# Optimization experiments

Hardware: AMD Instinct MI355X
Metric: run time of the kernel (lower is better)

## Reference

```python
import jax, jax.numpy as jnp
import numpy as np

# dims
B, T, D, H, DFF, NTYPE = 8, 1024, 512, 8, 1024, 341
HD = D // H                    # 64 head dim
NUM_AXES = 1
DPR = D // H // (NUM_AXES + 1) # 32 dims rotated per axis
EPS = 1e-5
THETA = 10000.0


def layernorm(x, g, b):
    m = jnp.mean(x, axis=-1, keepdims=True)
    v = jnp.mean((x - m) ** 2, axis=-1, keepdims=True)
    return (x - m) * jax.lax.rsqrt(v + EPS) * g + b


def swiglu(x):
    a, gate = jnp.split(x, 2, axis=-1)
    return jax.nn.silu(gate) * a


def apply_rope(x, pos):
    # x: [B,H,T,DPR], pos: [B,T] float positions (possibly non-integer / scrambled order)
    inv_freq = 1.0 / (THETA ** (jnp.arange(0, DPR, 2, dtype=jnp.float32) / DPR))  # [DPR/2]
    freqs = pos[:, None, :, None] * inv_freq          # [B,1,T,DPR/2]
    cos = jnp.repeat(jnp.cos(freqs), 2, axis=-1)      # each freq repeated twice -> [B,1,T,DPR]
    sin = jnp.repeat(jnp.sin(freqs), 2, axis=-1)
    x1 = x[..., 0::2]
    x2 = x[..., 1::2]
    rot = jnp.stack([-x2, x1], axis=-1).reshape(x.shape)  # rotate_half, interleaved pairs
    return x * cos + rot * sin


def setup_inputs() -> dict:
    key = jax.random.key(0)
    ks = jax.random.split(key, 16)
    s = lambda d: 1.0 / np.sqrt(d)
    return {
        "x_type": jax.random.randint(ks[0], (B, T + 1), 0, NTYPE),
        "x_value": jax.random.normal(ks[1], (B, T, D), dtype=jnp.float32),
        "seq_order": jax.random.uniform(ks[2], (B, T + 1), dtype=jnp.float32) * T,
        "W_attn": jax.random.normal(ks[3], (D, 3 * D), dtype=jnp.float32) * s(D),
        "type_emb": jax.random.normal(ks[4], (NTYPE, 2 * D), dtype=jnp.float32) * 0.02,
        "ln1_g": jnp.ones((D,), jnp.float32),
        "ln1_b": jnp.zeros((D,), jnp.float32),
        "ln2_g": jnp.ones((D,), jnp.float32),
        "ln2_b": jnp.zeros((D,), jnp.float32),
        "W1": jax.random.normal(ks[5], (D, 2 * DFF), dtype=jnp.float32) * s(D),
        "b1": jnp.zeros((2 * DFF,), jnp.float32),
        "W2": jax.random.normal(ks[6], (DFF, D), dtype=jnp.float32) * s(DFF),
        "b2": jnp.zeros((D,), jnp.float32),
    }


def reference(x_type, x_value, seq_order, W_attn, type_emb, ln1_g, ln1_b, ln2_g, ln2_b, W1, b1, W2, b2):
    # --- attention sublayer ---
    h = layernorm(x_value, ln1_g, ln1_b)                  # [B,T,D]
    qkv = h @ W_attn                                      # [B,T,3D]
    q, k, v = jnp.split(qkv, 3, axis=-1)
    emb = type_emb[x_type]                                # [B,T+1,2D]
    q_embed, k_embed = jnp.split(emb, 2, axis=-1)
    q = q + q_embed[:, :-1]
    k = k + k_embed[:, 1:]
    # [B,H,T,HD]
    to_heads = lambda t: t.reshape(B, T, H, HD).transpose(0, 2, 1, 3)
    q, k, v = to_heads(q), to_heads(k), to_heads(v)
    # rotate first DPR dims with (shifted) seq_order; remaining dims untouched
    q = jnp.concatenate([apply_rope(q[..., :DPR], seq_order[:, :-1]), q[..., DPR:]], axis=-1)
    k = jnp.concatenate([apply_rope(k[..., :DPR], seq_order[:, 1:]), k[..., DPR:]], axis=-1)
    # causal SDPA
    scores = jnp.einsum("bhqd,bhkd->bhqk", q, k) / jnp.sqrt(jnp.float32(HD))
    causal = jnp.tril(jnp.ones((T, T), dtype=bool))
    scores = jnp.where(causal, scores, -jnp.inf)
    attn = jax.nn.softmax(scores, axis=-1)
    out = jnp.einsum("bhqk,bhkd->bhqd", attn, v)          # [B,H,T,HD]
    out = out.transpose(0, 2, 1, 3).reshape(B, T, D)
    x = x_value + out
    # --- SwiGLU FFN sublayer ---
    h2 = layernorm(x, ln2_g, ln2_b)
    ff = swiglu(h2 @ W1 + b1) @ W2 + b2
    return x + ff
```

## Files before the change

### kernel.cpp

```cpp
#include <hip/hip_runtime.h>
#include <stdint.h>
#include <math.h>

typedef unsigned short u16;
typedef unsigned int u32;
typedef __attribute__((ext_vector_type(8))) short bf16x8;
typedef __attribute__((ext_vector_type(4))) float f32x4;
typedef __attribute__((ext_vector_type(2))) float f32x2;
typedef __attribute__((ext_vector_type(2))) u16 u16x2;
typedef __attribute__((ext_vector_type(8))) u16 u16x8;
typedef __attribute__((ext_vector_type(2))) u32 u32x2;

#define B_ 8
#define T_ 1024
#define D_ 512
#define H_ 8
#define TP1 1025
#define QSCALE 0.1803368801111204f

__device__ __forceinline__ u16 f2b(float f) {
  union { float f; u32 u; } v; v.f = f;
  return (u16)((v.u + 0x7fffu + ((v.u >> 16) & 1u)) >> 16);
}
__device__ __forceinline__ void gld16(const void* g, void* l) {
  __builtin_amdgcn_global_load_lds((const __attribute__((address_space(1))) u32*)g,
                                   (__attribute__((address_space(3))) u32*)l, 16, 0, 0);
}
__device__ __forceinline__ f32x4 mfma16(bf16x8 a, bf16x8 b, f32x4 c) {
  return __builtin_amdgcn_mfma_f32_16x16x32_bf16(a, b, c, 0, 0, 0);
}
__device__ __forceinline__ u32 cvtpk(float lo, float hi) {
  u32 r;
  asm("v_cvt_pk_bf16_f32 %0, %1, %2" : "=v"(r) : "v"(lo), "v"(hi));
  return r;
}
union U8 { u32 u[4]; bf16x8 v; };

#define WAITV(N) asm volatile("s_waitcnt vmcnt(" #N ")" ::: "memory")

__global__ __launch_bounds__(256) void prep_kernel(const float* __restrict__ W_attn,
    const float* __restrict__ W1, const float* __restrict__ W2,
    const float* __restrict__ seq,
    u16* __restrict__ WtA, u16* __restrict__ W1i, u16* __restrict__ W2t,
    float* __restrict__ cq, float* __restrict__ sq_,
    float* __restrict__ ck, float* __restrict__ sk,
    const float* __restrict__ xv, const float* __restrict__ ln1g,
    const float* __restrict__ ln1b, u16* __restrict__ hbuf) {
  int bid = blockIdx.x, tid = threadIdx.x;
  if (bid >= 1088) {
    int row = (bid - 1088) * 4 + (tid >> 6);
    int lane = tid & 63;
    const float* xr = xv + (size_t)row * D_ + lane * 8;
    f32x4 v0 = *(const f32x4*)xr;
    f32x4 v1 = *(const f32x4*)(xr + 4);
    float s = 0.f, sq = 0.f;
    #pragma unroll
    for (int j = 0; j < 4; j++) { s += v0[j] + v1[j]; sq += v0[j] * v0[j] + v1[j] * v1[j]; }
    #pragma unroll
    for (int m = 1; m < 64; m <<= 1) { s += __shfl_xor(s, m); sq += __shfl_xor(sq, m); }
    float mean = s * (1.f / D_);
    float var = sq * (1.f / D_) - mean * mean;
    float rstd = rsqrtf(var + 1e-5f);
    f32x4 g0 = *(const f32x4*)(ln1g + lane * 8);
    f32x4 g1 = *(const f32x4*)(ln1g + lane * 8 + 4);
    f32x4 b0 = *(const f32x4*)(ln1b + lane * 8);
    f32x4 b1 = *(const f32x4*)(ln1b + lane * 8 + 4);
    u16x8 o;
    #pragma unroll
    for (int j = 0; j < 4; j++) {
      o[j]     = f2b((v0[j] - mean) * rstd * g0[j] + b0[j]);
      o[4 + j] = f2b((v1[j] - mean) * rstd * g1[j] + b1[j]);
    }
    *(u16x8*)(hbuf + (size_t)row * D_ + lane * 8) = o;
    return;
  }
  if (bid >= 576) {
    int i = (bid - 576) * 256 + tid;
    int p = i & 15, bt = i >> 4, b = bt >> 10, t = bt & 1023;
    float inv = expf(-(float)p * 0.5756462732485115f);
    float aq = seq[b * TP1 + t] * inv;
    float ak = seq[b * TP1 + t + 1] * inv;
    cq[i] = cosf(aq); sq_[i] = sinf(aq);
    ck[i] = cosf(ak); sk[i] = sinf(ak);
    return;
  }
  __shared__ u16 lt[64][65];
  const float* src; u16* dst; int ld, Kd, k0, r0; bool ilv = false;
  if (bid < 192) {
    src = W_attn; dst = WtA; ld = 1536; Kd = 512;
    k0 = (bid & 7) * 64; r0 = (bid >> 3) * 64;
  } else if (bid < 448) {
    int t = bid - 192;
    src = W1; dst = W1i; ld = 2048; Kd = 512; ilv = true;
    k0 = (t & 7) * 64; r0 = (t >> 3) * 64;
  } else {
    int t = bid - 448;
    src = W2; dst = W2t; ld = 512; Kd = 1024;
    k0 = (t & 15) * 64; r0 = (t >> 4) * 64;
  }
  int nl = tid & 63;
  int scol, rloc;
  if (ilv) {
    if (nl < 32) { scol = (r0 >> 1) + nl;          rloc = ((nl >> 4) << 5) + (nl & 15); }
    else         { scol = 1024 + (r0 >> 1) + (nl - 32); rloc = (((nl - 32) >> 4) << 5) + 16 + (nl & 15); }
  } else { scol = r0 + nl; rloc = nl; }
  #pragma unroll
  for (int it = 0; it < 16; it++) {
    int kl = (tid >> 6) * 16 + it;
    lt[rloc][kl] = f2b(src[(size_t)(k0 + kl) * ld + scol]);
  }
  __syncthreads();
  #pragma unroll
  for (int it = 0; it < 16; it++) {
    int rl = (tid >> 6) * 16 + it;
    dst[(size_t)(r0 + rl) * Kd + k0 + nl] = lt[rl][nl];
  }
}

__global__ __launch_bounds__(256) void ln_kernel(const float* __restrict__ x,
    const float* __restrict__ g, const float* __restrict__ bta, u16* __restrict__ out) {
  int row = blockIdx.x * 4 + (threadIdx.x >> 6);
  int lane = threadIdx.x & 63;
  const float* xr = x + (size_t)row * D_ + lane * 8;
  f32x4 v0 = *(const f32x4*)xr;
  f32x4 v1 = *(const f32x4*)(xr + 4);
  float s = 0.f, sq = 0.f;
  #pragma unroll
  for (int j = 0; j < 4; j++) { s += v0[j] + v1[j]; sq += v0[j] * v0[j] + v1[j] * v1[j]; }
  #pragma unroll
  for (int m = 1; m < 64; m <<= 1) { s += __shfl_xor(s, m); sq += __shfl_xor(sq, m); }
  float mean = s * (1.f / D_);
  float var = sq * (1.f / D_) - mean * mean;
  float rstd = rsqrtf(var + 1e-5f);
  f32x4 g0 = *(const f32x4*)(g + lane * 8);
  f32x4 g1 = *(const f32x4*)(g + lane * 8 + 4);
  f32x4 b0 = *(const f32x4*)(bta + lane * 8);
  f32x4 b1 = *(const f32x4*)(bta + lane * 8 + 4);
  u16x8 o;
  #pragma unroll
  for (int j = 0; j < 4; j++) {
    o[j]     = f2b((v0[j] - mean) * rstd * g0[j] + b0[j]);
    o[4 + j] = f2b((v1[j] - mean) * rstd * g1[j] + b1[j]);
  }
  *(u16x8*)(out + (size_t)row * D_ + lane * 8) = o;
}

__global__ __launch_bounds__(256) void gemm_qkv(const u16* __restrict__ A,
    const u16* __restrict__ Bt,
    const int* __restrict__ x_type, const float* __restrict__ type_emb,
    const float* __restrict__ rqc, const float* __restrict__ rqs,
    const float* __restrict__ rkc, const float* __restrict__ rks,
    u16* __restrict__ qT, u16* __restrict__ kT, u16* __restrict__ vT) {
  __shared__ u16 lsmem[6 * 4096];
  u16* lA = lsmem;
  u16* lB = lsmem + 3 * 4096;
  const int K = 512, NK = 16;
  const int tid = threadIdx.x, lane = tid & 63, w = tid >> 6;
  const int wm = w >> 1, wn = w & 1;
  int swz = (blockIdx.x & 7) * 96 + (blockIdx.x >> 3);
  int byy = swz / 12, bxx = swz - byy * 12;
  const size_t bm = (size_t)byy * 128;
  const size_t bn = (size_t)bxx * 128;

  const int r0 = tid >> 2;
  const int cs = ((tid & 3) ^ ((r0 >> 1) & 3)) * 8;
  const u16* a0 = A + (bm + r0) * K + cs;
  const u16* a1 = A + (bm + 64 + r0) * K + cs;
  const u16* b0 = Bt + (bn + r0) * K + cs;
  const u16* b1p = Bt + (bn + 64 + r0) * K + cs;

  int aoff[4], boff[4];
  #pragma unroll
  for (int i = 0; i < 4; i++) {
    int ra = wm * 64 + i * 16 + (lane & 15);
    aoff[i] = ra * 64 + (((lane >> 4) ^ ((ra >> 1) & 3)) * 16);
    int rb = wn * 64 + i * 16 + (lane & 15);
    boff[i] = rb * 64 + (((lane >> 4) ^ ((rb >> 1) & 3)) * 16);
  }

  auto stage = [&](int j, int buf) {
    char* ad = (char*)lA + buf * 8192 + w * 1024;
    char* bd = (char*)lB + buf * 8192 + w * 1024;
    gld16(a0 + j * 32, ad);
    gld16(a1 + j * 32, ad + 4096);
    gld16(b0 + j * 32, bd);
    gld16(b1p + j * 32, bd + 4096);
  };
  f32x4 acc[4][4] = {};
  auto compute = [&](int buf) {
    const char* lAc = (const char*)lA + buf * 8192;
    const char* lBc = (const char*)lB + buf * 8192;
    bf16x8 af[4], bf[4];
    #pragma unroll
    for (int i = 0; i < 4; i++) af[i] = *(const bf16x8*)(lAc + aoff[i]);
    #pragma unroll
    for (int n = 0; n < 4; n++) bf[n] = *(const bf16x8*)(lBc + boff[n]);
    __builtin_amdgcn_s_setprio(1);
    #pragma unroll
    for (int i = 0; i < 4; i++)
      #pragma unroll
      for (int n = 0; n < 4; n++)
        acc[i][n] = mfma16(af[i], bf[n], acc[i][n]);
    __builtin_amdgcn_s_setprio(0);
  };

  stage(0, 0);
  stage(1, 1);
  int cur = 0;
  for (int j = 0; j < NK - 1; j++) {
    WAITV(4);
    __builtin_amdgcn_s_barrier();
    if (j + 2 < NK) { int nb = cur + 2; if (nb >= 3) nb -= 3; stage(j + 2, nb); }
    compute(cur);
    cur = (cur + 1 == 3) ? 0 : cur + 1;
  }
  WAITV(0);
  __builtin_amdgcn_s_barrier();
  compute(cur);

  const int region = (int)(bn >> 9);
  __syncthreads();
  u16 (*tbuf)[136] = (u16(*)[136])lsmem;
  const int bb = (int)(bm >> 10);
  const int t0 = (int)(bm & 1023);

  if (region < 2) {
    #pragma unroll
    for (int i = 0; i < 4; i++) {
      #pragma unroll
      for (int jj = 0; jj < 4; jj++) {
        int rl = wm * 64 + i * 16 + (lane >> 4) * 4 + jj;
        int row = (int)bm + rl;
        int b = row >> 10, t = row & 1023;
        int ty = x_type[b * TP1 + t + region];
        const float* rc = (region == 0) ? rqc : rkc;
        const float* rs = (region == 0) ? rqs : rks;
        #pragma unroll
        for (int n = 0; n < 4; n++) {
          int cl = wn * 64 + n * 16 + (lane & 15);
          int cloc = ((int)bn - region * 512) + cl;
          int hd = cloc & 63;
          float v = acc[i][n][jj] + type_emb[(size_t)ty * 1024 + region * 512 + cloc];
          float vp = __shfl_xor(v, 1);
          if (hd < 32) {
            int p = hd >> 1;
            float c = rc[row * 16 + p], s = rs[row * 16 + p];
            v = (hd & 1) ? (v * c + vp * s) : (v * c - vp * s);
          }
          if (region == 0) v *= QSCALE;
          tbuf[rl][cl] = f2b(v);
        }
      }
    }
    __syncthreads();
    u16* dst = (region == 0) ? qT : kT;
    const int h0 = (((int)bn - region * 512) >> 6);
    #pragma unroll
    for (int p = 0; p < 8; p++) {
      int chunk = p * 256 + tid;
      int tl = chunk >> 4;
      int cc = (chunk & 15) * 8;
      u16x8 o = *(const u16x8*)&tbuf[tl][cc];
      *(u16x8*)(dst + ((size_t)(bb * 8 + h0 + (cc >> 6)) * T_ + t0 + tl) * 64 +
                (cc & 63)) = o;
    }
  } else {
    #pragma unroll
    for (int i = 0; i < 4; i++) {
      #pragma unroll
      for (int n = 0; n < 4; n++) {
        int cl = wn * 64 + n * 16 + (lane & 15);
        #pragma unroll
        for (int jj = 0; jj < 4; jj++) {
          int r = wm * 64 + i * 16 + (lane >> 4) * 4 + jj;
          tbuf[cl][r] = f2b(acc[i][n][jj]);
        }
      }
    }
    __syncthreads();
    const int h0 = ((int)bn - 1024) >> 6;
    const size_t rbase = (size_t)(bb * 8 + h0) * 64;
    #pragma unroll
    for (int p = 0; p < 8; p++) {
      int rl = p * 16 + (tid >> 4);
      int c8 = (tid & 15) * 8;
      u16x8 o = *(const u16x8*)&tbuf[rl][c8];
      *(u16x8*)(vT + (rbase + rl) * T_ + t0 + c8) = o;
    }
  }
}

__global__ __launch_bounds__(512) void gemm_ff1(const u16* __restrict__ A,
    const u16* __restrict__ Bt, const float* __restrict__ b1,
    u16* __restrict__ outp) {
  __shared__ u16 lsmem[24576];
  u16* lA = lsmem;
  u16* lB = lsmem + 16384;
  const int K = 512;
  const int tid = threadIdx.x, lane = tid & 63, w = tid >> 6;
  const int wm = w >> 2, wn = w & 3;
  int swz = (blockIdx.x & 7) * 64 + (blockIdx.x >> 3);
  int byy = swz >> 4, bxx = swz & 15;
  const size_t bm = (size_t)byy * 256;
  const size_t bn = (size_t)bxx * 128;

  const int r0 = tid >> 2;
  const int cs = ((tid & 3) ^ ((r0 >> 1) & 3)) * 8;
  const u16* a0 = A + (bm + r0) * K + cs;
  const u16* a1 = A + (bm + 128 + r0) * K + cs;
  const u16* b0 = Bt + (bn + r0) * K + cs;

  int aoff[8], boff[2];
  #pragma unroll
  for (int i = 0; i < 8; i++) {
    int ra = wm * 128 + i * 16 + (lane & 15);
    aoff[i] = ra * 64 + (((lane >> 4) ^ ((ra >> 1) & 3)) * 16);
  }
  #pragma unroll
  for (int n = 0; n < 2; n++) {
    int rb = wn * 32 + n * 16 + (lane & 15);
    boff[n] = rb * 64 + (((lane >> 4) ^ ((rb >> 1) & 3)) * 16);
  }

  auto stage = [&](int k0, int buf) {
    char* ad = (char*)lA + buf * 16384 + w * 1024;
    char* bd = (char*)lB + buf * 8192 + w * 1024;
    gld16(a0 + k0, ad);
    gld16(a1 + k0, ad + 8192);
    gld16(b0 + k0, bd);
  };

  f32x4 acc[8][2] = {};
  stage(0, 0);
  __syncthreads();
  int cur = 0;
  for (int k0 = 0; k0 < K; k0 += 32) {
    if (k0 + 32 < K) stage(k0 + 32, cur ^ 1);
    const char* lAc = (const char*)lA + cur * 16384;
    const char* lBc = (const char*)lB + cur * 8192;
    bf16x8 bf[2];
    #pragma unroll
    for (int n = 0; n < 2; n++) bf[n] = *(const bf16x8*)(lBc + boff[n]);
    __builtin_amdgcn_s_setprio(1);
    #pragma unroll
    for (int i = 0; i < 8; i++) {
      bf16x8 af = *(const bf16x8*)(lAc + aoff[i]);
      acc[i][0] = mfma16(af, bf[0], acc[i][0]);
      acc[i][1] = mfma16(af, bf[1], acc[i][1]);
    }
    __builtin_amdgcn_s_setprio(0);
    __syncthreads();
    cur ^= 1;
  }
  __syncthreads();
  u16 (*tbuf)[72] = (u16(*)[72])lsmem;
  {
    int cl = wn * 16 + (lane & 15);
    int c = ((int)bn >> 1) + cl;
    float bav = b1[c], bgv = b1[1024 + c];
    #pragma unroll
    for (int i = 0; i < 8; i++) {
      #pragma unroll
      for (int jj = 0; jj < 4; jj++) {
        int rl = wm * 128 + i * 16 + (lane >> 4) * 4 + jj;
        float av = acc[i][0][jj] + bav;
        float gv = acc[i][1][jj] + bgv;
        float sg = gv / (1.f + expf(-gv));
        tbuf[rl][cl] = f2b(sg * av);
      }
    }
  }
  __syncthreads();
  {
    const int c0 = ((int)bn >> 1);
    #pragma unroll
    for (int p = 0; p < 4; p++) {
      int ch = p * 512 + tid;
      int rl = ch >> 3;
      int cc = (ch & 7) * 8;
      u16x8 o = *(const u16x8*)&tbuf[rl][cc];
      *(u16x8*)(outp + (size_t)((int)bm + rl) * 1024 + c0 + cc) = o;
    }
  }
}

__global__ __launch_bounds__(512) void gemm_ff2(const u16* __restrict__ A,
    const u16* __restrict__ Bt, const float* __restrict__ bias,
    float* __restrict__ C) {
  __shared__ u16 lA[2][8192];
  __shared__ u16 lB[2][8192];
  const int K = 1024, N = 512, NJ = 16;
  const int tid = threadIdx.x, lane = tid & 63, w = tid >> 6;
  const int wm = w >> 2, wn = w & 3;
  int swz = (blockIdx.x & 7) * 32 + (blockIdx.x >> 3);
  int byy = swz >> 2, bxx = swz & 3;
  const size_t bm = (size_t)byy * 128;
  const size_t bn = (size_t)bxx * 128;

  const int r0 = tid >> 2;
  const int cs = ((tid & 3) ^ ((r0 >> 1) & 3)) * 8;
  const u16* a0 = A + (bm + r0) * K + cs;
  const u16* b0 = Bt + (bn + r0) * K + cs;

  int aoff[4], boff[2];
  #pragma unroll
  for (int i = 0; i < 4; i++) {
    int ra = wm * 64 + i * 16 + (lane & 15);
    aoff[i] = ra * 64 + (((lane >> 4) ^ ((ra >> 1) & 3)) * 16);
  }
  #pragma unroll
  for (int n = 0; n < 2; n++) {
    int rb = wn * 32 + n * 16 + (lane & 15);
    boff[n] = rb * 64 + (((lane >> 4) ^ ((rb >> 1) & 3)) * 16);
  }

  auto stage = [&](int j, int buf) {
    #pragma unroll
    for (int kh = 0; kh < 2; kh++) {
      int ko = j * 64 + kh * 32;
      gld16(a0 + ko, (char*)lA + buf * 16384 + kh * 8192 + w * 1024);
      gld16(b0 + ko, (char*)lB + buf * 16384 + kh * 8192 + w * 1024);
    }
  };
  f32x4 acc[4][2] = {};
  auto compute = [&](int buf) {
    #pragma unroll
    for (int kh = 0; kh < 2; kh++) {
      const char* lAc = (const char*)lA + buf * 16384 + kh * 8192;
      const char* lBc = (const char*)lB + buf * 16384 + kh * 8192;
      bf16x8 af[4], bf[2];
      #pragma unroll
      for (int i = 0; i < 4; i++) af[i] = *(const bf16x8*)(lAc + aoff[i]);
      #pragma unroll
      for (int n = 0; n < 2; n++) bf[n] = *(const bf16x8*)(lBc + boff[n]);
      __builtin_amdgcn_s_setprio(1);
      #pragma unroll
      for (int i = 0; i < 4; i++)
        #pragma unroll
        for (int n = 0; n < 2; n++)
          acc[i][n] = mfma16(af[i], bf[n], acc[i][n]);
      __builtin_amdgcn_s_setprio(0);
    }
  };

  stage(0, 0);
  __syncthreads();
  int cur = 0;
  for (int j = 0; j < NJ; j++) {
    if (j + 1 < NJ) stage(j + 1, cur ^ 1);
    compute(cur);
    __syncthreads();
    cur ^= 1;
  }

  #pragma unroll
  for (int i = 0; i < 4; i++) {
    size_t mrow = bm + wm * 64 + i * 16 + (lane >> 4) * 4;
    #pragma unroll
    for (int n = 0; n < 2; n++) {
      size_t col = bn + wn * 32 + n * 16 + (lane & 15);
      float bv = bias[col];
      #pragma unroll
      for (int jj = 0; jj < 4; jj++) {
        size_t idx = (mrow + jj) * (size_t)N + col;
        C[idx] = acc[i][n][jj] + bv + C[idx];
      }
    }
  }
}

__global__ __launch_bounds__(512, 4) void attn_kernel(const u16* __restrict__ qT,
    const u16* __restrict__ kT, const u16* __restrict__ vT,
    const float* __restrict__ xv, float* __restrict__ X) {
  int s0 = (blockIdx.x & 7) * 64 + (blockIdx.x >> 3);
  const int bh = ((blockIdx.x & 7) << 3) + (s0 & 7);
  const int qp = 7 - ((s0 >> 3) & 7);
  const int b = bh >> 3, h = bh & 7;
  const int tid = threadIdx.x, lane = tid & 63, w = tid >> 6;
  const int q = lane & 15, g = lane >> 4;
  __shared__ u16 lK[2][8192];
  __shared__ u16 lV[2][8192];

  const int qrow0 = qp * 128 + w * 16;
  bf16x8 qf[2];
  {
    const u16* qp_ = qT + ((size_t)bh * T_ + qrow0 + q) * 64 + g * 8;
    qf[0] = *(const bf16x8*)qp_;
    qf[1] = *(const bf16x8*)(qp_ + 32);
  }
  f32x4 acc[4] = {};
  float mr = -1e30f, lr = 0.f;

  const int sr = tid >> 3;
  const int scs = ((tid & 7) ^ (sr & 7)) * 8;
  const u16* kb = kT + ((size_t)bh * T_ + sr) * 64 + scs;
  const u16* vb = vT + ((size_t)bh * 64 + sr) * T_ + scs;

  auto stage = [&](int j, int buf) {
    char* kd = (char*)lK + buf * 16384 + w * 1024;
    char* vd = (char*)lV + buf * 16384 + w * 1024;
    gld16(kb + (size_t)j * 8192, kd);
    gld16(kb + (size_t)j * 8192 + 4096, kd + 8192);
    gld16(vb + j * 128, vd);
    gld16(vb + j * 128 + 64, vd + 8192);
  };

  const int jmax = qp + 1;
  stage(0, 0);
  __syncthreads();
  int cur = 0;
  for (int j = 0; j < jmax; j++) {
    if (j + 1 < jmax) stage(j + 1, cur ^ 1);
    const char* lKc = (const char*)lK + cur * 16384;
    const char* lVc = (const char*)lV + cur * 16384;

    f32x4 s[8] = {};
    __builtin_amdgcn_s_setprio(1);
    #pragma unroll
    for (int ka = 0; ka < 2; ka++) {
      #pragma unroll
      for (int n = 0; n < 8; n++) {
        bf16x8 kf = *(const bf16x8*)(lKc + (n >> 2) * 8192 + ((n & 3) * 16 + q) * 128 +
                                     (((ka * 4 + g) ^ (q & 7)) * 16));
        s[n] = mfma16(kf, qf[ka], s[n]);
      }
    }
    __builtin_amdgcn_s_setprio(0);
    if (j == jmax - 1) {
      int qrow = w * 16 + q;
      #pragma unroll
      for (int n = 0; n < 8; n++)
        #pragma unroll
        for (int i = 0; i < 4; i++)
          if (n * 16 + g * 4 + i > qrow) s[n][i] = -1e30f;
    }
    float mt = -1e30f;
    #pragma unroll
    for (int n = 0; n < 8; n++)
      mt = fmaxf(mt, fmaxf(fmaxf(s[n][0], s[n][1]), fmaxf(s[n][2], s[n][3])));
    mt = fmaxf(mt, __shfl_xor(mt, 16));
    mt = fmaxf(mt, __shfl_xor(mt, 32));
    if (__any(mt > mr + 8.f)) {
      float mnew = fmaxf(mr, mt);
      float sc = exp2f(mr - mnew);
      mr = mnew;
      lr *= sc;
      #pragma unroll
      for (int t = 0; t < 4; t++) acc[t] *= sc;
    }
    float ps = 0.f;
    U8 pa[4];
    #pragma unroll
    for (int kt = 0; kt < 4; kt++) {
      float p0[4], p1[4];
      #pragma unroll
      for (int i = 0; i < 4; i++) {
        p0[i] = exp2f(s[2 * kt][i] - mr);
        p1[i] = exp2f(s[2 * kt + 1][i] - mr);
        ps += p0[i] + p1[i];
      }
      pa[kt].u[0] = cvtpk(p0[0], p0[1]);
      pa[kt].u[1] = cvtpk(p0[2], p0[3]);
      pa[kt].u[2] = cvtpk(p1[0], p1[1]);
      pa[kt].u[3] = cvtpk(p1[2], p1[3]);
    }
    ps += __shfl_xor(ps, 16);
    ps += __shfl_xor(ps, 32);
    lr += ps;
    __builtin_amdgcn_s_setprio(1);
    #pragma unroll
    for (int t = 0; t < 4; t++) {
      #pragma unroll
      for (int kt = 0; kt < 4; kt++) {
        const char* vrh = lVc + (kt >> 1) * 8192 + (t * 16 + q) * 128 + (g & 1) * 8;
        int ktl = kt & 1;
        u32x2 lo = *(const u32x2*)(vrh + (((ktl * 4 + (g >> 1)) ^ (q & 7)) * 16));
        u32x2 hi = *(const u32x2*)(vrh + (((ktl * 4 + 2 + (g >> 1)) ^ (q & 7)) * 16));
        U8 af;
        af.u[0] = lo[0]; af.u[1] = lo[1]; af.u[2] = hi[0]; af.u[3] = hi[1];
        acc[t] = mfma16(af.v, pa[kt].v, acc[t]);
      }
    }
    __builtin_amdgcn_s_setprio(0);
    __syncthreads();
    cur ^= 1;
  }
  {
    float inv = 1.f / lr;
    size_t base = ((size_t)b * T_ + qrow0 + q) * D_ + h * 64 + g * 4;
    #pragma unroll
    for (int t = 0; t < 4; t++) {
      f32x4 r = *(const f32x4*)(xv + base + t * 16);
      f32x4 o;
      #pragma unroll
      for (int i = 0; i < 4; i++) o[i] = r[i] + acc[t][i] * inv;
      *(f32x4*)(X + base + t * 16) = o;
    }
  }
}

extern "C" void kernel_launch(void* const* d_in, const int* in_sizes, int n_in,
                              void* d_out, int out_size, void* d_ws, size_t ws_size,
                              hipStream_t stream) {
  const int*   x_type   = (const int*)d_in[0];
  const float* x_value  = (const float*)d_in[1];
  const float* seq      = (const float*)d_in[2];
  const float* W_attn   = (const float*)d_in[3];
  const float* type_emb = (const float*)d_in[4];
  const float* ln1_g    = (const float*)d_in[5];
  const float* ln1_b    = (const float*)d_in[6];
  const float* ln2_g    = (const float*)d_in[7];
  const float* ln2_b    = (const float*)d_in[8];
  const float* W1       = (const float*)d_in[9];
  const float* b1       = (const float*)d_in[10];
  const float* W2       = (const float*)d_in[11];
  const float* b2       = (const float*)d_in[12];
  float* out = (float*)d_out;
  char* ws = (char*)d_ws;

  u16*   WtA  = (u16*)(ws + 0);
  u16*   W1i  = (u16*)(ws + 1572864);
  u16*   W2t  = (u16*)(ws + 3670016);
  float* rqc  = (float*)(ws + 4718592);
  float* rqs  = (float*)(ws + 5242880);
  float* rkc  = (float*)(ws + 5767168);
  float* rks  = (float*)(ws + 6291456);
  u16*   hbuf = (u16*)(ws + 6815744);
  u16*   qTb  = (u16*)(ws + 15204352);
  u16*   kTb  = (u16*)(ws + 23592960);
  u16*   vTb  = (u16*)(ws + 31981568);
  u16*   ff1a = (u16*)(ws + 15204352);

  prep_kernel<<<3136, 256, 0, stream>>>(W_attn, W1, W2, seq, WtA, W1i, W2t,
                                        rqc, rqs, rkc, rks,
                                        x_value, ln1_g, ln1_b, hbuf);
  gemm_qkv<<<768, 256, 0, stream>>>(hbuf, WtA, x_type, type_emb,
                                    rqc, rqs, rkc, rks, qTb, kTb, vTb);
  attn_kernel<<<512, 512, 0, stream>>>(qTb, kTb, vTb, x_value, out);
  ln_kernel<<<B_ * T_ / 4, 256, 0, stream>>>(out, ln2_g, ln2_b, hbuf);
  gemm_ff1<<<512, 512, 0, stream>>>(hbuf, W1i, b1, ff1a);
  gemm_ff2<<<256, 512, 0, stream>>>(ff1a, W2t, b2, out);
}
```

Measured before the change: 116.1 us.

## Restructure QKV GEMM to 8 waves with double-buffered K=64 stages

The QKV projection GEMM moves from 4 waves (each computing a 64x64 sub-tile) to 8 waves (each computing 64x32) per 128x128 block. The K loop changes from a 3-stage pipeline of 32-wide slices with vmcnt waits to a 2-buffer pipeline of 64-wide slices synchronised by __syncthreads. The aim is more waves per CU to hide latency and half as many loop iterations. In exchange, each wave has fewer MFMAs per LDS load, LDS grows to 64KB, and full barriers replace the finer-grained waits.

```diff
diff --git a/kernel.cpp b/kernel.cpp
--- a/kernel.cpp
+++ b/kernel.cpp
@@ -145,18 +145,18 @@
   *(u16x8*)(out + (size_t)row * D_ + lane * 8) = o;
 }
 
-__global__ __launch_bounds__(256) void gemm_qkv(const u16* __restrict__ A,
+__global__ __launch_bounds__(512) void gemm_qkv(const u16* __restrict__ A,
     const u16* __restrict__ Bt,
     const int* __restrict__ x_type, const float* __restrict__ type_emb,
     const float* __restrict__ rqc, const float* __restrict__ rqs,
     const float* __restrict__ rkc, const float* __restrict__ rks,
     u16* __restrict__ qT, u16* __restrict__ kT, u16* __restrict__ vT) {
-  __shared__ u16 lsmem[6 * 4096];
+  __shared__ u16 lsmem[32768];
   u16* lA = lsmem;
-  u16* lB = lsmem + 3 * 4096;
-  const int K = 512, NK = 16;
+  u16* lB = lsmem + 16384;
+  const int K = 512, NJ = 8;
   const int tid = threadIdx.x, lane = tid & 63, w = tid >> 6;
-  const int wm = w >> 1, wn = w & 1;
+  const int wm = w >> 2, wn = w & 3;
   int swz = (blockIdx.x & 7) * 96 + (blockIdx.x >> 3);
   int byy = swz / 12, bxx = swz - byy * 12;
   const size_t bm = (size_t)byy * 128;
@@ -165,58 +165,58 @@
   const int r0 = tid >> 2;
   const int cs = ((tid & 3) ^ ((r0 >> 1) & 3)) * 8;
   const u16* a0 = A + (bm + r0) * K + cs;
-  const u16* a1 = A + (bm + 64 + r0) * K + cs;
   const u16* b0 = Bt + (bn + r0) * K + cs;
-  const u16* b1p = Bt + (bn + 64 + r0) * K + cs;
-
-  int aoff[4], boff[4];
+
+  int aoff[4], boff[2];
   #pragma unroll
   for (int i = 0; i < 4; i++) {
     int ra = wm * 64 + i * 16 + (lane & 15);
     aoff[i] = ra * 64 + (((lane >> 4) ^ ((ra >> 1) & 3)) * 16);
-    int rb = wn * 64 + i * 16 + (lane & 15);
-    boff[i] = rb * 64 + (((lane >> 4) ^ ((rb >> 1) & 3)) * 16);
+  }
+  #pragma unroll
+  for (int n = 0; n < 2; n++) {
+    int rb = wn * 32 + n * 16 + (lane & 15);
+    boff[n] = rb * 64 + (((lane >> 4) ^ ((rb >> 1) & 3)) * 16);
   }
 
   auto stage = [&](int j, int buf) {
-    char* ad = (char*)lA + buf * 8192 + w * 1024;
-    char* bd = (char*)lB + buf * 8192 + w * 1024;
-    gld16(a0 + j * 32, ad);
-    gld16(a1 + j * 32, ad + 4096);
-    gld16(b0 + j * 32, bd);
-    gld16(b1p + j * 32, bd + 4096);
+    #pragma unroll
+    for (int kh = 0; kh < 2; kh++) {
+      int ko = j * 64 + kh * 32;
+      gld16(a0 + ko, (char*)lA + buf * 16384 + kh * 8192 + w * 1024);
+      gld16(b0 + ko, (char*)lB + buf * 16384 + kh * 8192 + w * 1024);
+    }
   };
-  f32x4 acc[4][4] = {};
+  f32x4 acc[4][2] = {};
   auto compute = [&](int buf) {
-    const char* lAc = (const char*)lA + buf * 8192;
-    const char* lBc = (const char*)lB + buf * 8192;
-    bf16x8 af[4], bf[4];
-    #pragma unroll
-    for (int i = 0; i < 4; i++) af[i] = *(const bf16x8*)(lAc + aoff[i]);
-    #pragma unroll
-    for (int n = 0; n < 4; n++) bf[n] = *(const bf16x8*)(lBc + boff[n]);
-    __builtin_amdgcn_s_setprio(1);
-    #pragma unroll
-    for (int i = 0; i < 4; i++)
-      #pragma unroll
-      for (int n = 0; n < 4; n++)
-        acc[i][n] = mfma16(af[i], bf[n], acc[i][n]);
-    __builtin_amdgcn_s_setprio(0);
+    #pragma unroll
+    for (int kh = 0; kh < 2; kh++) {
+      const char* lAc = (const char*)lA + buf * 16384 + kh * 8192;
+      const char* lBc = (const char*)lB + buf * 16384 + kh * 8192;
+      bf16x8 af[4], bf[2];
+      #pragma unroll
+      for (int i = 0; i < 4; i++) af[i] = *(const bf16x8*)(lAc + aoff[i]);
+      #pragma unroll
+      for (int n = 0; n < 2; n++) bf[n] = *(const bf16x8*)(lBc + boff[n]);
+      __builtin_amdgcn_s_setprio(1);
+      #pragma unroll
+      for (int i = 0; i < 4; i++)
+        #pragma unroll
+        for (int n = 0; n < 2; n++)
+          acc[i][n] = mfma16(af[i], bf[n], acc[i][n]);
+      __builtin_amdgcn_s_setprio(0);
+    }
   };
 
   stage(0, 0);
-  stage(1, 1);
+  __syncthreads();
   int cur = 0;
-  for (int j = 0; j < NK - 1; j++) {
-    WAITV(4);
-    __builtin_amdgcn_s_barrier();
-    if (j + 2 < NK) { int nb = cur + 2; if (nb >= 3) nb -= 3; stage(j + 2, nb); }
+  for (int j = 0; j < NJ; j++) {
+    if (j + 1 < NJ) stage(j + 1, cur ^ 1);
     compute(cur);
-    cur = (cur + 1 == 3) ? 0 : cur + 1;
-  }
-  WAITV(0);
-  __builtin_amdgcn_s_barrier();
-  compute(cur);
+    __syncthreads();
+    cur ^= 1;
+  }
 
   const int region = (int)(bn >> 9);
   __syncthreads();
@@ -236,8 +236,8 @@
         const float* rc = (region == 0) ? rqc : rkc;
         const float* rs = (region == 0) ? rqs : rks;
         #pragma unroll
-        for (int n = 0; n < 4; n++) {
-          int cl = wn * 64 + n * 16 + (lane & 15);
+        for (int n = 0; n < 2; n++) {
+          int cl = wn * 32 + n * 16 + (lane & 15);
           int cloc = ((int)bn - region * 512) + cl;
           int hd = cloc & 63;
           float v = acc[i][n][jj] + type_emb[(size_t)ty * 1024 + region * 512 + cloc];
@@ -256,8 +256,8 @@
     u16* dst = (region == 0) ? qT : kT;
     const int h0 = (((int)bn - region * 512) >> 6);
     #pragma unroll
-    for (int p = 0; p < 8; p++) {
-      int chunk = p * 256 + tid;
+    for (int p = 0; p < 4; p++) {
+      int chunk = p * 512 + tid;
       int tl = chunk >> 4;
       int cc = (chunk & 15) * 8;
       u16x8 o = *(const u16x8*)&tbuf[tl][cc];
@@ -268,8 +268,8 @@
     #pragma unroll
     for (int i = 0; i < 4; i++) {
       #pragma unroll
-      for (int n = 0; n < 4; n++) {
-        int cl = wn * 64 + n * 16 + (lane & 15);
+      for (int n = 0; n < 2; n++) {
+        int cl = wn * 32 + n * 16 + (lane & 15);
         #pragma unroll
         for (int jj = 0; jj < 4; jj++) {
           int r = wm * 64 + i * 16 + (lane >> 4) * 4 + jj;
@@ -281,8 +281,8 @@
     const int h0 = ((int)bn - 1024) >> 6;
     const size_t rbase = (size_t)(bb * 8 + h0) * 64;
     #pragma unroll
-    for (int p = 0; p < 8; p++) {
-      int rl = p * 16 + (tid >> 4);
+    for (int p = 0; p < 4; p++) {
+      int rl = p * 32 + (tid >> 4);
       int c8 = (tid & 15) * 8;
       u16x8 o = *(const u16x8*)&tbuf[rl][c8];
       *(u16x8*)(vT + (rbase + rl) * T_ + t0 + c8) = o;
@@ -634,7 +634,7 @@
   prep_kernel<<<3136, 256, 0, stream>>>(W_attn, W1, W2, seq, WtA, W1i, W2t,
                                         rqc, rqs, rkc, rks,
                                         x_value, ln1_g, ln1_b, hbuf);
-  gemm_qkv<<<768, 256, 0, stream>>>(hbuf, WtA, x_type, type_emb,
+  gemm_qkv<<<768, 512, 0, stream>>>(hbuf, WtA, x_type, type_emb,
                                     rqc, rqs, rkc, rks, qTb, kTb, vTb);
   attn_kernel<<<512, 512, 0, stream>>>(qTb, kTb, vTb, x_value, out);
   ln_kernel<<<B_ * T_ / 4, 256, 0, stream>>>(out, ln2_g, ln2_b, hbuf);
```

After: 129.6 us. 11.7% more time.
